# Performance work log

Hardware: AMD Instinct MI355X
Metric: run time of the kernel (lower is better)

## Reference

```python
import jax, jax.numpy as jnp
import numpy as np
import math

VOCAB = 50257
BLOCK = 2048
NE = 768


def setup_inputs() -> dict:
    key = jax.random.key(0)
    ks = jax.random.split(key, 12)
    s = 0.02
    idx = jax.random.randint(ks[0], (4, 2048), 0, VOCAB, dtype=jnp.int64 if jax.config.jax_enable_x64 else jnp.int32)
    tok_emb = jax.random.normal(ks[1], (VOCAB, NE), jnp.float32) * s
    pos_emb = jax.random.normal(ks[2], (BLOCK, NE), jnp.float32) * s
    Wk = jax.random.normal(ks[3], (NE, NE), jnp.float32) * s
    bk = jnp.zeros((NE,), jnp.float32)
    Wq = jax.random.normal(ks[4], (NE, NE), jnp.float32) * s
    bq = jnp.zeros((NE,), jnp.float32)
    Wv = jax.random.normal(ks[5], (NE, NE), jnp.float32) * s
    bv = jnp.zeros((NE,), jnp.float32)
    ln_g = jnp.ones((NE,), jnp.float32)
    ln_b = jnp.zeros((NE,), jnp.float32)
    Wh = jax.random.normal(ks[6], (NE, VOCAB), jnp.float32) * s
    bh = jnp.zeros((VOCAB,), jnp.float32)
    return {"idx": idx, "tok_emb": tok_emb, "pos_emb": pos_emb, "Wq": Wq, "bq": bq,
            "Wk": Wk, "bk": bk, "Wv": Wv, "bv": bv, "ln_g": ln_g, "ln_b": ln_b,
            "Wh": Wh, "bh": bh}


def reference(idx, tok_emb, pos_emb, Wq, bq, Wk, bk, Wv, bv, ln_g, ln_b, Wh, bh):
    B, T = idx.shape
    C = tok_emb.shape[1]
    x = tok_emb[idx] + pos_emb[:T]  # [B,T,C]
    q = jnp.einsum('btc,cd->btd', x, Wq) + bq
    k = jnp.einsum('btc,cd->btd', x, Wk) + bk
    v = jnp.einsum('btc,cd->btd', x, Wv) + bv
    att = jnp.einsum('btd,bsd->bts', q, k) / math.sqrt(C)  # [B,T,T]
    causal = jnp.tril(jnp.ones((T, T), bool))
    att = jnp.where(causal, att, -jnp.inf)
    att = jax.nn.softmax(att, axis=-1)
    y = jnp.einsum('bts,bsd->btd', att, v)
    # LayerNorm (eps=1e-5, torch default)
    mu = jnp.mean(y, axis=-1, keepdims=True)
    var = jnp.mean((y - mu) ** 2, axis=-1, keepdims=True)
    yn = (y - mu) * jax.lax.rsqrt(var + 1e-5) * ln_g + ln_b
    logits = jnp.einsum('btc,cv->btv', yn, Wh) + bh
    return logits
```

## Files before the change

### kernel.cpp

```cpp
#include <hip/hip_runtime.h>
#include <hip/hip_bf16.h>
#include <math.h>

typedef __bf16 bf16x8 __attribute__((ext_vector_type(8)));
typedef float  f32x4  __attribute__((ext_vector_type(4)));

#define GAS(p) ((const __attribute__((address_space(1))) void*)(p))
#define LAS(p) ((__attribute__((address_space(3))) void*)(p))

static constexpr int NE = 768;

__global__ __launch_bounds__(256) void k_embed(const int* __restrict__ idx,
    const float* __restrict__ tok, const float* __restrict__ pos,
    __hip_bfloat16* __restrict__ xb)
{
    int bt = blockIdx.x;
    int t  = bt & 2047;
    int token = idx[bt];
    const float* te = tok + (size_t)token * NE;
    const float* pe = pos + (size_t)t * NE;
    __hip_bfloat16* o = xb + (size_t)bt * NE;
    for (int c = threadIdx.x; c < NE; c += 256)
        o[c] = __float2bfloat16(te[c] + pe[c]);
}

__global__ __launch_bounds__(256) void k_transpose_f32_bf16(
    const float* __restrict__ in, __hip_bfloat16* __restrict__ out,
    int R, int C, int outRows)
{
    __shared__ float tile[32][33];
    int c0 = blockIdx.x * 32, r0 = blockIdx.y * 32;
    int tx = threadIdx.x & 31, ty = threadIdx.x >> 5;
    #pragma unroll
    for (int i = 0; i < 32; i += 8) {
        int r = r0 + ty + i, c = c0 + tx;
        tile[ty + i][tx] = (r < R && c < C) ? in[(size_t)r * C + c] : 0.f;
    }
    __syncthreads();
    #pragma unroll
    for (int i = 0; i < 32; i += 8) {
        int oc = c0 + ty + i, orr = r0 + tx;
        if (oc < outRows && orr < R)
            out[(size_t)oc * R + orr] = __float2bfloat16(tile[tx][ty + i]);
    }
}

__global__ __launch_bounds__(256) void k_transpose_bf16(
    const __hip_bfloat16* __restrict__ in, __hip_bfloat16* __restrict__ out,
    int R, int C)
{
    __shared__ __hip_bfloat16 tile[32][33];
    size_t boff = (size_t)blockIdx.z * R * C;
    int c0 = blockIdx.x * 32, r0 = blockIdx.y * 32;
    int tx = threadIdx.x & 31, ty = threadIdx.x >> 5;
    #pragma unroll
    for (int i = 0; i < 32; i += 8)
        tile[ty + i][tx] = in[boff + (size_t)(r0 + ty + i) * C + (c0 + tx)];
    __syncthreads();
    #pragma unroll
    for (int i = 0; i < 32; i += 8)
        out[boff + (size_t)(c0 + ty + i) * R + (r0 + tx)] = tile[tx][ty + i];
}

__global__ __launch_bounds__(256) void k_pack_bias(const float* __restrict__ bq,
    const float* __restrict__ bk, const float* __restrict__ bv, float* __restrict__ o)
{
    int i = blockIdx.x * 256 + threadIdx.x;
    if (i < 768) o[i] = bq[i];
    else if (i < 1536) o[i] = bk[i - 768];
    else if (i < 2304) o[i] = bv[i - 1536];
}

template<int MODE>
__global__ __launch_bounds__(256) void k_gemm(
    const __hip_bfloat16* __restrict__ A, const __hip_bfloat16* __restrict__ Bt,
    int K, int lda, int ldb,
    size_t strideA, size_t strideB, size_t strideC,
    float* __restrict__ outf, int ldc, int ncols,
    const float* __restrict__ bias, float scale,
    __hip_bfloat16* __restrict__ oq, __hip_bfloat16* __restrict__ ok,
    __hip_bfloat16* __restrict__ ov)
{
    int bn = blockIdx.x, bm = blockIdx.y, bz = blockIdx.z;
    if constexpr (MODE == 2) bm = (int)gridDim.y - 1 - bm;
    if (MODE == 1 && bn > bm) return;
    __shared__ __align__(16) __hip_bfloat16 As[128 * 32];
    __shared__ __align__(16) __hip_bfloat16 Bs[128 * 32];
    const __hip_bfloat16* Ab = A  + bz * strideA + (size_t)bm * 128 * lda;
    const __hip_bfloat16* Bb = Bt + bz * strideB + (size_t)bn * 128 * ldb;
    int tid = threadIdx.x, w = tid >> 6, lane = tid & 63;
    int wr = w >> 1, wc = w & 1;
    f32x4 acc[4][4] = {};
    int sr = tid >> 2, sc = (tid & 3) * 8;
    int lr = lane & 15, lk = (lane >> 4) * 8;

    const int kend = (MODE == 2) ? (bm + 1) * 128 : K;

    for (int k0 = 0; k0 < kend; k0 += 32) {
        __syncthreads();
        #pragma unroll
        for (int i = 0; i < 2; ++i) {
            __builtin_amdgcn_global_load_lds(GAS(Ab + (size_t)(i * 64 + sr) * lda + k0 + sc),
                                             LAS((char*)As + i * 4096 + w * 1024), 16, 0, 0);
            __builtin_amdgcn_global_load_lds(GAS(Bb + (size_t)(i * 64 + sr) * ldb + k0 + sc),
                                             LAS((char*)Bs + i * 4096 + w * 1024), 16, 0, 0);
        }
        __syncthreads();
        bf16x8 af[4], bfv[4];
        #pragma unroll
        for (int mi = 0; mi < 4; ++mi)
            af[mi] = *(const bf16x8*)(As + (wr * 64 + mi * 16 + lr) * 32 + lk);
        #pragma unroll
        for (int ni = 0; ni < 4; ++ni)
            bfv[ni] = *(const bf16x8*)(Bs + (wc * 64 + ni * 16 + lr) * 32 + lk);
        #pragma unroll
        for (int mi = 0; mi < 4; ++mi)
            #pragma unroll
            for (int ni = 0; ni < 4; ++ni)
                acc[mi][ni] = __builtin_amdgcn_mfma_f32_16x16x32_bf16(af[mi], bfv[ni], acc[mi][ni], 0, 0, 0);
    }

    int r4 = (lane >> 4) * 4;
    #pragma unroll
    for (int mi = 0; mi < 4; ++mi) {
        #pragma unroll
        for (int ni = 0; ni < 4; ++ni) {
            #pragma unroll
            for (int r = 0; r < 4; ++r) {
                int row = bm * 128 + wr * 64 + mi * 16 + r4 + r;
                int col = bn * 128 + wc * 64 + ni * 16 + lr;
                float v = acc[mi][ni][r];
                if constexpr (MODE == 0) {
                    v += bias[col];
                    __hip_bfloat16 h = __float2bfloat16(v);
                    if (col < 768)       oq[(size_t)row * 768 + col]          = h;
                    else if (col < 1536) ok[(size_t)row * 768 + (col - 768)]  = h;
                    else                 ov[(size_t)row * 768 + (col - 1536)] = h;
                } else if constexpr (MODE == 1) {
                    outf[bz * strideC + (size_t)row * ldc + col] = v * scale;
                } else {
                    outf[bz * strideC + (size_t)row * ldc + col] = v;
                }
            }
        }
    }
}

__global__ __launch_bounds__(512, 2) void k_gemm_head(
    const __hip_bfloat16* __restrict__ A,
    const __hip_bfloat16* __restrict__ Bt,
    float* __restrict__ out, const float* __restrict__ bias, int ldc, int ncols)
{
    constexpr int K = 768, NT = K / 64;
    __shared__ __align__(16) __hip_bfloat16 As[2][256 * 64];
    __shared__ __align__(16) __hip_bfloat16 Bs[2][256 * 64];

    const int Nx = (int)gridDim.x;
    const int qq = Nx >> 3, rr = Nx & 7;
    const int xcd = (int)blockIdx.x & 7, xidx = (int)blockIdx.x >> 3;
    const int bn = (xcd < rr ? xcd * (qq + 1) : rr * (qq + 1) + (xcd - rr) * qq) + xidx;
    const int bm = blockIdx.y;
    const int tid = threadIdx.x;
    const int w = tid >> 6, lane = tid & 63;
    const int wr = w >> 2, wc = w & 3;
    const int lr = lane & 15, lu = lane >> 4;
    const int rswz = lr & 7;

    const int srow = tid >> 3;
    const int sunit = (tid & 7) ^ (srow & 7);
    const size_t Abase = (size_t)bm * 256 * K;
    const size_t Bbase = (size_t)bn * 256 * K;

    auto stageA = [&](int kt, int c, int p) {
        const __hip_bfloat16* src = A + Abase + (size_t)(c * 64 + srow) * K + kt * 64 + sunit * 8;
        __builtin_amdgcn_global_load_lds(GAS(src), LAS(&As[p][c * 4096 + tid * 8]), 16, 0, 0);
    };
    auto stageB = [&](int kt, int c, int p) {
        const __hip_bfloat16* src = Bt + Bbase + (size_t)(c * 64 + srow) * K + kt * 64 + sunit * 8;
        __builtin_amdgcn_global_load_lds(GAS(src), LAS(&Bs[p][c * 4096 + tid * 8]), 16, 0, 0);
    };
    auto rdA = [&](int p, int m, int kk) {
        return *(const bf16x8*)&As[p][(wr * 128 + m * 16 + lr) * 64 + ((kk * 4 + lu) ^ rswz) * 8];
    };
    auto rdB = [&](int p, int n, int kk) {
        return *(const bf16x8*)&Bs[p][(wc * 64 + n * 16 + lr) * 64 + ((kk * 4 + lu) ^ rswz) * 8];
    };

    f32x4 acc[8][4] = {};

    stageB(0, 0, 0); stageB(0, 1, 0); stageB(0, 2, 0); stageB(0, 3, 0);
    stageA(0, 0, 0); stageA(0, 1, 0); stageA(0, 2, 0); stageA(0, 3, 0);
    stageB(1, 0, 1); stageB(1, 1, 1); stageB(1, 2, 1); stageB(1, 3, 1);
    stageA(1, 0, 1); stageA(1, 2, 1);

#define QUAD(Q)                                                                                          \
    {   bf16x8 a00 = rdA(p, 2*(Q),     0), a01 = rdA(p, 2*(Q),     1);                                   \
        bf16x8 a10 = rdA(p, 2*(Q) + 1, 0), a11 = rdA(p, 2*(Q) + 1, 1);                                   \
        __builtin_amdgcn_s_setprio(1);                                                                   \
        _Pragma("unroll")                                                                                \
        for (int n = 0; n < 4; ++n) {                                                                    \
            acc[2*(Q)][n]     = __builtin_amdgcn_mfma_f32_16x16x32_bf16(a00, bf[n][0], acc[2*(Q)][n],     0, 0, 0); \
            acc[2*(Q)][n]     = __builtin_amdgcn_mfma_f32_16x16x32_bf16(a01, bf[n][1], acc[2*(Q)][n],     0, 0, 0); \
            acc[2*(Q) + 1][n] = __builtin_amdgcn_mfma_f32_16x16x32_bf16(a10, bf[n][0], acc[2*(Q) + 1][n], 0, 0, 0); \
            acc[2*(Q) + 1][n] = __builtin_amdgcn_mfma_f32_16x16x32_bf16(a11, bf[n][1], acc[2*(Q) + 1][n], 0, 0, 0); \
        }                                                                                                \
        __builtin_amdgcn_s_setprio(0); }

    for (int kt = 0; kt < NT; ++kt) {
        const int p = kt & 1, pn = p ^ 1;
        if (kt + 1 < NT) {
            stageA(kt + 1, 1, pn); stageA(kt + 1, 3, pn);
            asm volatile("s_waitcnt vmcnt(8)" ::: "memory");
        } else {
            asm volatile("s_waitcnt vmcnt(0)" ::: "memory");
        }
        asm volatile("s_barrier" ::: "memory");
        bf16x8 bf[4][2];
        #pragma unroll
        for (int n = 0; n < 4; ++n) { bf[n][0] = rdB(p, n, 0); bf[n][1] = rdB(p, n, 1); }
        QUAD(0)
        asm volatile("s_barrier" ::: "memory");
        if (kt + 2 < NT) { stageB(kt + 2, 0, p); stageB(kt + 2, 1, p); }
        QUAD(1)
        asm volatile("s_barrier" ::: "memory");
        if (kt + 2 < NT) { stageB(kt + 2, 2, p); stageB(kt + 2, 3, p); }
        QUAD(2)
        asm volatile("s_barrier" ::: "memory");
        if (kt + 2 < NT) { stageA(kt + 2, 0, p); stageA(kt + 2, 2, p); }
        QUAD(3)
        asm volatile("s_barrier" ::: "memory");
    }
#undef QUAD

    const int r4 = lu * 4;
    #pragma unroll
    for (int m = 0; m < 8; ++m) {
        #pragma unroll
        for (int n = 0; n < 4; ++n) {
            int col = bn * 256 + wc * 64 + n * 16 + lr;
            if (col < ncols) {
                float bv_ = bias[col];
                #pragma unroll
                for (int r = 0; r < 4; ++r) {
                    int row = bm * 256 + wr * 128 + m * 16 + r4 + r;
                    out[(size_t)row * ldc + col] = acc[m][n][r] + bv_;
                }
            }
        }
    }
}

__global__ __launch_bounds__(256) void k_softmax(const float* __restrict__ att,
    __hip_bfloat16* __restrict__ P, int T)
{
    int t = blockIdx.x, b = blockIdx.y;
    const float* row = att + ((size_t)b * T + t) * T;
    __hip_bfloat16* prow = P + ((size_t)b * T + t) * T;
    const int n = t + 1;
    const int nz = ((t >> 7) + 1) << 7;
    __shared__ float red[256];
    float4 v[2];
    float mx = -1e30f;
    #pragma unroll
    for (int j = 0; j < 2; ++j) {
        int e = (threadIdx.x + j * 256) * 4;
        v[j] = *(const float4*)(row + e);
        #pragma unroll
        for (int k = 0; k < 4; ++k)
            if (e + k < n) mx = fmaxf(mx, ((const float*)&v[j])[k]);
    }
    red[threadIdx.x] = mx; __syncthreads();
    for (int o = 128; o > 0; o >>= 1) {
        if (threadIdx.x < o) red[threadIdx.x] = fmaxf(red[threadIdx.x], red[threadIdx.x + o]);
        __syncthreads();
    }
    mx = red[0]; __syncthreads();
    float ev[8];
    float sum = 0.f;
    #pragma unroll
    for (int j = 0; j < 2; ++j) {
        int e = (threadIdx.x + j * 256) * 4;
        #pragma unroll
        for (int k = 0; k < 4; ++k) {
            float x = ((const float*)&v[j])[k];
            float ex = (e + k < n) ? __expf(x - mx) : 0.f;
            ev[j * 4 + k] = ex;
            sum += ex;
        }
    }
    red[threadIdx.x] = sum; __syncthreads();
    for (int o = 128; o > 0; o >>= 1) {
        if (threadIdx.x < o) red[threadIdx.x] += red[threadIdx.x + o];
        __syncthreads();
    }
    float inv = 1.f / red[0];
    #pragma unroll
    for (int j = 0; j < 2; ++j) {
        int e = (threadIdx.x + j * 256) * 4;
        #pragma unroll
        for (int k = 0; k < 4; ++k)
            if (e + k < nz) prow[e + k] = __float2bfloat16(ev[j * 4 + k] * inv);
    }
}

__global__ __launch_bounds__(256) void k_layernorm(const float* __restrict__ y,
    const float* __restrict__ g, const float* __restrict__ b,
    __hip_bfloat16* __restrict__ yn)
{
    int row = blockIdx.x;
    const float* yr = y + (size_t)row * NE;
    float s = 0.f, s2 = 0.f;
    for (int c = threadIdx.x; c < NE; c += 256) { float v = yr[c]; s += v; s2 += v * v; }
    __shared__ float r1[256], r2[256];
    r1[threadIdx.x] = s; r2[threadIdx.x] = s2; __syncthreads();
    for (int o = 128; o > 0; o >>= 1) {
        if (threadIdx.x < o) { r1[threadIdx.x] += r1[threadIdx.x + o]; r2[threadIdx.x] += r2[threadIdx.x + o]; }
        __syncthreads();
    }
    float mu = r1[0] / NE;
    float var = r2[0] / NE - mu * mu;
    float rs = rsqrtf(var + 1e-5f);
    __hip_bfloat16* o = yn + (size_t)row * NE;
    for (int c = threadIdx.x; c < NE; c += 256)
        o[c] = __float2bfloat16((yr[c] - mu) * rs * g[c] + b[c]);
}

extern "C" void kernel_launch(void* const* d_in, const int* in_sizes, int n_in,
                              void* d_out, int out_size, void* d_ws, size_t ws_size,
                              hipStream_t stream)
{
    const int*   idx  = (const int*)  d_in[0];
    const float* tok  = (const float*)d_in[1];
    const float* pos  = (const float*)d_in[2];
    const float* Wq   = (const float*)d_in[3];
    const float* bq   = (const float*)d_in[4];
    const float* Wk   = (const float*)d_in[5];
    const float* bk   = (const float*)d_in[6];
    const float* Wv   = (const float*)d_in[7];
    const float* bv   = (const float*)d_in[8];
    const float* ln_g = (const float*)d_in[9];
    const float* ln_b = (const float*)d_in[10];
    const float* Wh   = (const float*)d_in[11];
    const float* bh   = (const float*)d_in[12];
    float* out = (float*)d_out;

    const int B = 4, T = 2048, C = 768, V = 50257, Vp = 50432;

    char* p = (char*)d_ws;
    auto take = [&](size_t bytes) { char* r = p; p += (bytes + 255) & ~(size_t)255; return r; };
    __hip_bfloat16* xb    = (__hip_bfloat16*)take((size_t)B * T * C * 2);
    __hip_bfloat16* wqkvT = (__hip_bfloat16*)take((size_t)3 * C * C * 2);
    float*          bqkv  = (float*)take((size_t)3 * C * 4);
    __hip_bfloat16* qb    = (__hip_bfloat16*)take((size_t)B * T * C * 2);
    __hip_bfloat16* kb    = (__hip_bfloat16*)take((size_t)B * T * C * 2);
    __hip_bfloat16* vb    = (__hip_bfloat16*)take((size_t)B * T * C * 2);
    __hip_bfloat16* vT    = (__hip_bfloat16*)take((size_t)B * T * C * 2);
    float*          att   = (float*)take((size_t)B * T * T * 4);
    __hip_bfloat16* P     = (__hip_bfloat16*)take((size_t)B * T * T * 2);
    float*          y     = (float*)take((size_t)B * T * C * 4);
    __hip_bfloat16* yn    = (__hip_bfloat16*)take((size_t)B * T * C * 2);
    __hip_bfloat16* whT   = (__hip_bfloat16*)att;

    float scale = 1.0f / sqrtf((float)C);

    k_embed<<<dim3(B * T), 256, 0, stream>>>(idx, tok, pos, xb);
    k_transpose_f32_bf16<<<dim3(24, 24), 256, 0, stream>>>(Wq, wqkvT,             C, C, C);
    k_transpose_f32_bf16<<<dim3(24, 24), 256, 0, stream>>>(Wk, wqkvT + C * C,     C, C, C);
    k_transpose_f32_bf16<<<dim3(24, 24), 256, 0, stream>>>(Wv, wqkvT + 2 * C * C, C, C, C);
    k_pack_bias<<<dim3(9), 256, 0, stream>>>(bq, bk, bv, bqkv);

    k_gemm<0><<<dim3(18, 64, 1), 256, 0, stream>>>(xb, wqkvT, C, C, C, 0, 0, 0,
        nullptr, 0, 0, bqkv, 1.f, qb, kb, vb);

    k_transpose_bf16<<<dim3(24, 64, B), 256, 0, stream>>>(vb, vT, T, C);

    k_gemm<1><<<dim3(16, 16, B), 256, 0, stream>>>(qb, kb, C, C, C,
        (size_t)T * C, (size_t)T * C, (size_t)T * T, att, T, 0, nullptr, scale,
        nullptr, nullptr, nullptr);

    k_softmax<<<dim3(T, B), 256, 0, stream>>>(att, P, T);

    k_gemm<2><<<dim3(6, 16, B), 256, 0, stream>>>(P, vT, T, T, T,
        (size_t)T * T, (size_t)C * T, (size_t)T * C, y, C, 0, nullptr, 1.f,
        nullptr, nullptr, nullptr);

    k_transpose_f32_bf16<<<dim3(Vp / 32, 24), 256, 0, stream>>>(Wh, whT, C, V, Vp);

    k_layernorm<<<dim3(B * T), 256, 0, stream>>>(y, ln_g, ln_b, yn);

    k_gemm_head<<<dim3(Vp / 256, 32), 512, 0, stream>>>(yn, whT, out, bh, V, V);
}
```

Baseline: 1.274 ms.

## Restructure head GEMM into 8-phase ping-pong pipeline with half-tile LDS staging

Rewrites the LM-head GEMM main loop to process two K-tiles per iteration in eight phases. Each phase issues part of the next global-to-LDS loads, reads A fragments, and runs an MFMA cluster between barriers. LDS tiles are split into 128-row halves that map to each wave's row or column group, and the MFMA order inside each cluster changes. The aim is to overlap memory staging with compute more evenly and cut waitcnt stalls, at the cost of more barriers and a more fragile schedule.

```diff
diff --git a/kernel.cpp b/kernel.cpp
--- a/kernel.cpp
+++ b/kernel.cpp
@@ -151,9 +151,9 @@
     const __hip_bfloat16* __restrict__ Bt,
     float* __restrict__ out, const float* __restrict__ bias, int ldc, int ncols)
 {
-    constexpr int K = 768, NT = K / 64;
-    __shared__ __align__(16) __hip_bfloat16 As[2][256 * 64];
-    __shared__ __align__(16) __hip_bfloat16 Bs[2][256 * 64];
+    constexpr int K = 768, NT = K / 64, NI = NT / 2;
+    __shared__ __align__(16) __hip_bfloat16 As[2][2][128 * 64];
+    __shared__ __align__(16) __hip_bfloat16 Bs[2][2][128 * 64];
 
     const int Nx = (int)gridDim.x;
     const int qq = Nx >> 3, rr = Nx & 7;
@@ -164,73 +164,89 @@
     const int w = tid >> 6, lane = tid & 63;
     const int wr = w >> 2, wc = w & 3;
     const int lr = lane & 15, lu = lane >> 4;
-    const int rswz = lr & 7;
-
-    const int srow = tid >> 3;
-    const int sunit = (tid & 7) ^ (srow & 7);
-    const size_t Abase = (size_t)bm * 256 * K;
-    const size_t Bbase = (size_t)bn * 256 * K;
-
-    auto stageA = [&](int kt, int c, int p) {
-        const __hip_bfloat16* src = A + Abase + (size_t)(c * 64 + srow) * K + kt * 64 + sunit * 8;
-        __builtin_amdgcn_global_load_lds(GAS(src), LAS(&As[p][c * 4096 + tid * 8]), 16, 0, 0);
+
+    const int sr = tid >> 3;
+    const int su = (tid & 7) ^ (sr & 7);
+    const __hip_bfloat16* Ap = A  + (size_t)(bm * 256) * K;
+    const __hip_bfloat16* Bp = Bt + (size_t)(bn * 256) * K;
+
+    f32x4 acc[8][4] = {};
+    bf16x8 bq[4][2];
+
+    auto stageAh = [&](int t, int h) {
+        #pragma unroll
+        for (int l = 0; l < 2; ++l)
+            __builtin_amdgcn_global_load_lds(
+                GAS(Ap + (size_t)(h * 128 + l * 64 + sr) * K + t * 64 + su * 8),
+                LAS(&As[t & 1][h][l * 4096 + tid * 8]), 16, 0, 0);
     };
-    auto stageB = [&](int kt, int c, int p) {
-        const __hip_bfloat16* src = Bt + Bbase + (size_t)(c * 64 + srow) * K + kt * 64 + sunit * 8;
-        __builtin_amdgcn_global_load_lds(GAS(src), LAS(&Bs[p][c * 4096 + tid * 8]), 16, 0, 0);
+    auto stageBh = [&](int t, int h) {
+        #pragma unroll
+        for (int l = 0; l < 2; ++l)
+            __builtin_amdgcn_global_load_lds(
+                GAS(Bp + (size_t)(h * 128 + l * 64 + sr) * K + t * 64 + su * 8),
+                LAS(&Bs[t & 1][h][l * 4096 + tid * 8]), 16, 0, 0);
     };
-    auto rdA = [&](int p, int m, int kk) {
-        return *(const bf16x8*)&As[p][(wr * 128 + m * 16 + lr) * 64 + ((kk * 4 + lu) ^ rswz) * 8];
+    auto rdA = [&](int b, int q, int f, int kk) {
+        int row = q * 32 + f * 16 + lr;
+        return *(const bf16x8*)&As[b][wr][row * 64 + (((kk * 4 + lu) ^ (row & 7)) << 3)];
     };
-    auto rdB = [&](int p, int n, int kk) {
-        return *(const bf16x8*)&Bs[p][(wc * 64 + n * 16 + lr) * 64 + ((kk * 4 + lu) ^ rswz) * 8];
+    auto rdB = [&](int b, int n, int kk) {
+        int row = (wc & 1) * 64 + n * 16 + lr;
+        return *(const bf16x8*)&Bs[b][wc >> 1][row * 64 + (((kk * 4 + lu) ^ (row & 7)) << 3)];
     };
 
-    f32x4 acc[8][4] = {};
-
-    stageB(0, 0, 0); stageB(0, 1, 0); stageB(0, 2, 0); stageB(0, 3, 0);
-    stageA(0, 0, 0); stageA(0, 1, 0); stageA(0, 2, 0); stageA(0, 3, 0);
-    stageB(1, 0, 1); stageB(1, 1, 1); stageB(1, 2, 1); stageB(1, 3, 1);
-    stageA(1, 0, 1); stageA(1, 2, 1);
-
-#define QUAD(Q)                                                                                          \
-    {   bf16x8 a00 = rdA(p, 2*(Q),     0), a01 = rdA(p, 2*(Q),     1);                                   \
-        bf16x8 a10 = rdA(p, 2*(Q) + 1, 0), a11 = rdA(p, 2*(Q) + 1, 1);                                   \
-        __builtin_amdgcn_s_setprio(1);                                                                   \
-        _Pragma("unroll")                                                                                \
-        for (int n = 0; n < 4; ++n) {                                                                    \
-            acc[2*(Q)][n]     = __builtin_amdgcn_mfma_f32_16x16x32_bf16(a00, bf[n][0], acc[2*(Q)][n],     0, 0, 0); \
-            acc[2*(Q)][n]     = __builtin_amdgcn_mfma_f32_16x16x32_bf16(a01, bf[n][1], acc[2*(Q)][n],     0, 0, 0); \
-            acc[2*(Q) + 1][n] = __builtin_amdgcn_mfma_f32_16x16x32_bf16(a10, bf[n][0], acc[2*(Q) + 1][n], 0, 0, 0); \
-            acc[2*(Q) + 1][n] = __builtin_amdgcn_mfma_f32_16x16x32_bf16(a11, bf[n][1], acc[2*(Q) + 1][n], 0, 0, 0); \
-        }                                                                                                \
-        __builtin_amdgcn_s_setprio(0); }
-
-    for (int kt = 0; kt < NT; ++kt) {
-        const int p = kt & 1, pn = p ^ 1;
-        if (kt + 1 < NT) {
-            stageA(kt + 1, 1, pn); stageA(kt + 1, 3, pn);
-            asm volatile("s_waitcnt vmcnt(8)" ::: "memory");
-        } else {
-            asm volatile("s_waitcnt vmcnt(0)" ::: "memory");
-        }
-        asm volatile("s_barrier" ::: "memory");
-        bf16x8 bf[4][2];
-        #pragma unroll
-        for (int n = 0; n < 4; ++n) { bf[n][0] = rdB(p, n, 0); bf[n][1] = rdB(p, n, 1); }
-        QUAD(0)
-        asm volatile("s_barrier" ::: "memory");
-        if (kt + 2 < NT) { stageB(kt + 2, 0, p); stageB(kt + 2, 1, p); }
-        QUAD(1)
-        asm volatile("s_barrier" ::: "memory");
-        if (kt + 2 < NT) { stageB(kt + 2, 2, p); stageB(kt + 2, 3, p); }
-        QUAD(2)
-        asm volatile("s_barrier" ::: "memory");
-        if (kt + 2 < NT) { stageA(kt + 2, 0, p); stageA(kt + 2, 2, p); }
-        QUAD(3)
-        asm volatile("s_barrier" ::: "memory");
-    }
-#undef QUAD
+#define BAR() asm volatile("s_barrier" ::: "memory")
+#define VM4() asm volatile("s_waitcnt vmcnt(4)" ::: "memory")
+#define VM0() asm volatile("s_waitcnt vmcnt(0)" ::: "memory")
+#define CLUSTER(Q)                                                                                          \
+    __builtin_amdgcn_s_setprio(1);                                                                          \
+    _Pragma("unroll") for (int n = 0; n < 4; ++n)                                                           \
+        acc[2*(Q)+0][n] = __builtin_amdgcn_mfma_f32_16x16x32_bf16(af[0][0], bq[n][0], acc[2*(Q)+0][n], 0, 0, 0); \
+    _Pragma("unroll") for (int n = 0; n < 4; ++n)                                                           \
+        acc[2*(Q)+1][n] = __builtin_amdgcn_mfma_f32_16x16x32_bf16(af[1][0], bq[n][0], acc[2*(Q)+1][n], 0, 0, 0); \
+    _Pragma("unroll") for (int n = 0; n < 4; ++n)                                                           \
+        acc[2*(Q)+0][n] = __builtin_amdgcn_mfma_f32_16x16x32_bf16(af[0][1], bq[n][1], acc[2*(Q)+0][n], 0, 0, 0); \
+    _Pragma("unroll") for (int n = 0; n < 4; ++n)                                                           \
+        acc[2*(Q)+1][n] = __builtin_amdgcn_mfma_f32_16x16x32_bf16(af[1][1], bq[n][1], acc[2*(Q)+1][n], 0, 0, 0); \
+    __builtin_amdgcn_s_setprio(0);
+#define PH(B_, Q_, STAGE, VM)                                                   \
+    {   bf16x8 af[2][2];                                                        \
+        _Pragma("unroll") for (int f = 0; f < 2; ++f) {                         \
+            af[f][0] = rdA(B_, Q_, f, 0); af[f][1] = rdA(B_, Q_, f, 1); }       \
+        STAGE                                                                   \
+        VM                                                                      \
+        BAR();                                                                  \
+        CLUSTER(Q_)                                                             \
+        BAR(); }
+
+    stageBh(0, 0); stageBh(0, 1);
+    stageAh(0, 0); stageAh(0, 1);
+    stageBh(1, 0); stageBh(1, 1);
+    VM0();
+    BAR();
+
+    for (int i = 0; i < NI; ++i) {
+        const int t0 = 2 * i, t1 = 2 * i + 1;
+        const bool full = (i + 1 < NI);
+        #pragma unroll
+        for (int n = 0; n < 4; ++n) { bq[n][0] = rdB(0, n, 0); bq[n][1] = rdB(0, n, 1); }
+        PH(0, 0, stageAh(t1, 0); stageAh(t1, 1);, )
+        PH(0, 1, if (full) { stageBh(t0 + 2, 0); }, )
+        PH(0, 2, if (full) { stageBh(t0 + 2, 1); }, )
+        PH(0, 3, , if (full) { VM4(); } else { VM0(); })
+        #pragma unroll
+        for (int n = 0; n < 4; ++n) { bq[n][0] = rdB(1, n, 0); bq[n][1] = rdB(1, n, 1); }
+        PH(1, 0, if (full) { stageAh(t0 + 2, 0); }, )
+        PH(1, 1, if (full) { stageAh(t0 + 2, 1); }, )
+        PH(1, 2, if (full) { stageBh(t1 + 2, 0); }, )
+        PH(1, 3, if (full) { stageBh(t1 + 2, 1); }, if (full) { VM4(); } else { VM0(); })
+    }
+#undef PH
+#undef CLUSTER
+#undef VM0
+#undef VM4
+#undef BAR
 
     const int r4 = lu * 4;
     #pragma unroll
```

After: 1.239 ms. -2.8%, faster.

## Make head GEMM persistent over four M-tiles with a 4-stage K=32 pipeline

Applied to the files above, without the earlier changes.

Each head-GEMM workgroup now walks four consecutive 256-row M tiles for one N tile, so the grid shrinks from 32 to 8 rows of blocks. The K step drops from 64 to 32 with a 4-slot LDS ring kept three stages ahead, using a new XOR swizzle. The pipeline runs continuously across tile boundaries, with the epilogue and accumulator reset done inline. The aim is to hide load latency and amortise pipeline fill across tiles. In exchange there are fewer blocks and more barriers per unit of MFMA work, and the epilogue stores now sit in the main loop.

```diff
diff --git a/kernel.cpp b/kernel.cpp
--- a/kernel.cpp
+++ b/kernel.cpp
@@ -151,103 +151,132 @@
     const __hip_bfloat16* __restrict__ Bt,
     float* __restrict__ out, const float* __restrict__ bias, int ldc, int ncols)
 {
-    constexpr int K = 768, NT = K / 64;
-    __shared__ __align__(16) __hip_bfloat16 As[2][256 * 64];
-    __shared__ __align__(16) __hip_bfloat16 Bs[2][256 * 64];
+    constexpr int K = 768, KT = K / 32;
+    constexpr int TILES = 4, NSTEP = KT * TILES;
+    __shared__ __align__(16) __hip_bfloat16 As[4][256 * 32];
+    __shared__ __align__(16) __hip_bfloat16 Bs[4][256 * 32];
 
     const int Nx = (int)gridDim.x;
     const int qq = Nx >> 3, rr = Nx & 7;
     const int xcd = (int)blockIdx.x & 7, xidx = (int)blockIdx.x >> 3;
     const int bn = (xcd < rr ? xcd * (qq + 1) : rr * (qq + 1) + (xcd - rr) * qq) + xidx;
-    const int bm = blockIdx.y;
+    const int grp = blockIdx.y;
     const int tid = threadIdx.x;
     const int w = tid >> 6, lane = tid & 63;
     const int wr = w >> 2, wc = w & 3;
     const int lr = lane & 15, lu = lane >> 4;
-    const int rswz = lr & 7;
-
-    const int srow = tid >> 3;
-    const int sunit = (tid & 7) ^ (srow & 7);
-    const size_t Abase = (size_t)bm * 256 * K;
-    const size_t Bbase = (size_t)bn * 256 * K;
-
-    auto stageA = [&](int kt, int c, int p) {
-        const __hip_bfloat16* src = A + Abase + (size_t)(c * 64 + srow) * K + kt * 64 + sunit * 8;
-        __builtin_amdgcn_global_load_lds(GAS(src), LAS(&As[p][c * 4096 + tid * 8]), 16, 0, 0);
+
+    const __hip_bfloat16* Bp = Bt + (size_t)(bn * 256) * K;
+
+    f32x4 acc[8][4] = {};
+    bf16x8 bq[4];
+
+    auto stageA = [&](int ws) {
+        int bm = grp * 4 + (ws / KT);
+        int kt = ws - (ws / KT) * KT;
+        const __hip_bfloat16* base = A + (size_t)(bm * 256) * K + kt * 32;
+        #pragma unroll
+        for (int l = 0; l < 2; ++l) {
+            int v = l * 512 + tid;
+            int row = v >> 2, uc = v & 3;
+            int s = (row ^ (row >> 2)) & 3;
+            __builtin_amdgcn_global_load_lds(GAS(base + (size_t)row * K + ((uc ^ s) << 3)),
+                                             LAS(&As[ws & 3][v * 8]), 16, 0, 0);
+        }
     };
-    auto stageB = [&](int kt, int c, int p) {
-        const __hip_bfloat16* src = Bt + Bbase + (size_t)(c * 64 + srow) * K + kt * 64 + sunit * 8;
-        __builtin_amdgcn_global_load_lds(GAS(src), LAS(&Bs[p][c * 4096 + tid * 8]), 16, 0, 0);
+    auto stageB = [&](int ws) {
+        int kt = ws - (ws / KT) * KT;
+        const __hip_bfloat16* base = Bp + kt * 32;
+        #pragma unroll
+        for (int l = 0; l < 2; ++l) {
+            int v = l * 512 + tid;
+            int row = v >> 2, uc = v & 3;
+            int s = (row ^ (row >> 2)) & 3;
+            __builtin_amdgcn_global_load_lds(GAS(base + (size_t)row * K + ((uc ^ s) << 3)),
+                                             LAS(&Bs[ws & 3][v * 8]), 16, 0, 0);
+        }
     };
-    auto rdA = [&](int p, int m, int kk) {
-        return *(const bf16x8*)&As[p][(wr * 128 + m * 16 + lr) * 64 + ((kk * 4 + lu) ^ rswz) * 8];
+    auto rdA = [&](int sl, int mh, int f) {
+        int row = wr * 128 + mh * 64 + f * 16 + lr;
+        int s = (row ^ (row >> 2)) & 3;
+        return *(const bf16x8*)&As[sl][row * 32 + ((lu ^ s) << 3)];
     };
-    auto rdB = [&](int p, int n, int kk) {
-        return *(const bf16x8*)&Bs[p][(wc * 64 + n * 16 + lr) * 64 + ((kk * 4 + lu) ^ rswz) * 8];
+    auto rdB = [&](int sl, int n) {
+        int row = wc * 64 + n * 16 + lr;
+        int s = (row ^ (row >> 2)) & 3;
+        return *(const bf16x8*)&Bs[sl][row * 32 + ((lu ^ s) << 3)];
     };
 
-    f32x4 acc[8][4] = {};
-
-    stageB(0, 0, 0); stageB(0, 1, 0); stageB(0, 2, 0); stageB(0, 3, 0);
-    stageA(0, 0, 0); stageA(0, 1, 0); stageA(0, 2, 0); stageA(0, 3, 0);
-    stageB(1, 0, 1); stageB(1, 1, 1); stageB(1, 2, 1); stageB(1, 3, 1);
-    stageA(1, 0, 1); stageA(1, 2, 1);
-
-#define QUAD(Q)                                                                                          \
-    {   bf16x8 a00 = rdA(p, 2*(Q),     0), a01 = rdA(p, 2*(Q),     1);                                   \
-        bf16x8 a10 = rdA(p, 2*(Q) + 1, 0), a11 = rdA(p, 2*(Q) + 1, 1);                                   \
-        __builtin_amdgcn_s_setprio(1);                                                                   \
-        _Pragma("unroll")                                                                                \
-        for (int n = 0; n < 4; ++n) {                                                                    \
-            acc[2*(Q)][n]     = __builtin_amdgcn_mfma_f32_16x16x32_bf16(a00, bf[n][0], acc[2*(Q)][n],     0, 0, 0); \
-            acc[2*(Q)][n]     = __builtin_amdgcn_mfma_f32_16x16x32_bf16(a01, bf[n][1], acc[2*(Q)][n],     0, 0, 0); \
-            acc[2*(Q) + 1][n] = __builtin_amdgcn_mfma_f32_16x16x32_bf16(a10, bf[n][0], acc[2*(Q) + 1][n], 0, 0, 0); \
-            acc[2*(Q) + 1][n] = __builtin_amdgcn_mfma_f32_16x16x32_bf16(a11, bf[n][1], acc[2*(Q) + 1][n], 0, 0, 0); \
-        }                                                                                                \
-        __builtin_amdgcn_s_setprio(0); }
-
-    for (int kt = 0; kt < NT; ++kt) {
-        const int p = kt & 1, pn = p ^ 1;
-        if (kt + 1 < NT) {
-            stageA(kt + 1, 1, pn); stageA(kt + 1, 3, pn);
-            asm volatile("s_waitcnt vmcnt(8)" ::: "memory");
-        } else {
-            asm volatile("s_waitcnt vmcnt(0)" ::: "memory");
-        }
-        asm volatile("s_barrier" ::: "memory");
-        bf16x8 bf[4][2];
-        #pragma unroll
-        for (int n = 0; n < 4; ++n) { bf[n][0] = rdB(p, n, 0); bf[n][1] = rdB(p, n, 1); }
-        QUAD(0)
-        asm volatile("s_barrier" ::: "memory");
-        if (kt + 2 < NT) { stageB(kt + 2, 0, p); stageB(kt + 2, 1, p); }
-        QUAD(1)
-        asm volatile("s_barrier" ::: "memory");
-        if (kt + 2 < NT) { stageB(kt + 2, 2, p); stageB(kt + 2, 3, p); }
-        QUAD(2)
-        asm volatile("s_barrier" ::: "memory");
-        if (kt + 2 < NT) { stageA(kt + 2, 0, p); stageA(kt + 2, 2, p); }
-        QUAD(3)
-        asm volatile("s_barrier" ::: "memory");
-    }
-#undef QUAD
-
-    const int r4 = lu * 4;
-    #pragma unroll
-    for (int m = 0; m < 8; ++m) {
-        #pragma unroll
-        for (int n = 0; n < 4; ++n) {
-            int col = bn * 256 + wc * 64 + n * 16 + lr;
-            if (col < ncols) {
-                float bv_ = bias[col];
+#define BAR() asm volatile("s_barrier" ::: "memory")
+
+    stageA(0); stageB(0); stageA(1); stageB(1); stageA(2); stageB(2);
+    asm volatile("s_waitcnt vmcnt(8)" ::: "memory");
+    BAR();
+
+    for (int u = 0; u < NSTEP; ++u) {
+        const int sl = u & 3;
+        #pragma unroll
+        for (int n = 0; n < 4; ++n) bq[n] = rdB(sl, n);
+        {
+            bf16x8 af[4];
+            #pragma unroll
+            for (int f = 0; f < 4; ++f) af[f] = rdA(sl, 0, f);
+            if (u + 3 < NSTEP) stageA(u + 3);
+            BAR();
+            __builtin_amdgcn_s_setprio(1);
+            #pragma unroll
+            for (int n = 0; n < 4; ++n)
                 #pragma unroll
-                for (int r = 0; r < 4; ++r) {
-                    int row = bm * 256 + wr * 128 + m * 16 + r4 + r;
-                    out[(size_t)row * ldc + col] = acc[m][n][r] + bv_;
+                for (int f = 0; f < 4; ++f)
+                    acc[f][n] = __builtin_amdgcn_mfma_f32_16x16x32_bf16(af[f], bq[n], acc[f][n], 0, 0, 0);
+            __builtin_amdgcn_s_setprio(0);
+            BAR();
+        }
+        {
+            bf16x8 af[4];
+            #pragma unroll
+            for (int f = 0; f < 4; ++f) af[f] = rdA(sl, 1, f);
+            if (u + 3 < NSTEP) {
+                stageB(u + 3);
+                asm volatile("s_waitcnt vmcnt(8)" ::: "memory");
+            } else if (u + 2 < NSTEP) {
+                asm volatile("s_waitcnt vmcnt(4)" ::: "memory");
+            } else if (u + 1 < NSTEP) {
+                asm volatile("s_waitcnt vmcnt(0)" ::: "memory");
+            }
+            BAR();
+            __builtin_amdgcn_s_setprio(1);
+            #pragma unroll
+            for (int n = 0; n < 4; ++n)
+                #pragma unroll
+                for (int f = 0; f < 4; ++f)
+                    acc[4 + f][n] = __builtin_amdgcn_mfma_f32_16x16x32_bf16(af[f], bq[n], acc[4 + f][n], 0, 0, 0);
+            __builtin_amdgcn_s_setprio(0);
+            BAR();
+        }
+        if (((u + 1) % KT) == 0) {
+            const int bm = grp * 4 + (u / KT);
+            const int r4 = lu * 4;
+            #pragma unroll
+            for (int m = 0; m < 8; ++m) {
+                #pragma unroll
+                for (int n = 0; n < 4; ++n) {
+                    int col = bn * 256 + wc * 64 + n * 16 + lr;
+                    if (col < ncols) {
+                        float bv_ = bias[col];
+                        #pragma unroll
+                        for (int r = 0; r < 4; ++r) {
+                            int row = bm * 256 + wr * 128 + m * 16 + r4 + r;
+                            out[(size_t)row * ldc + col] = acc[m][n][r] + bv_;
+                        }
+                    }
+                    #pragma unroll
+                    for (int r = 0; r < 4; ++r) acc[m][n][r] = 0.f;
                 }
             }
         }
     }
+#undef BAR
 }
 
 __global__ __launch_bounds__(256) void k_softmax(const float* __restrict__ att,
@@ -388,5 +417,5 @@
 
     k_layernorm<<<dim3(B * T), 256, 0, stream>>>(y, ln_g, ln_b, yn);
 
-    k_gemm_head<<<dim3(Vp / 256, 32), 512, 0, stream>>>(yn, whT, out, bh, V, V);
-}
+    k_gemm_head<<<dim3(197, 8), 512, 0, stream>>>(yn, whT, out, bh, V, V);
+}
```

New measurement: 1.422 ms. 11.6% more time.
